# Optimization experiments

Hardware: AMD Instinct MI355X
Metric: run time of the kernel (lower is better)

The kernel has to match this reference:

```python
import jax, jax.numpy as jnp
import numpy as np

N, M, D_IN, H1, D, OUT_C = 2048, 128, 352, 512, 256, 13


def _lin_bn_relu(x, w, b, g, be):
    # 1x1 conv == linear over last dim; BN (eval) folded to per-channel affine (g, be)
    return jax.nn.relu(g * (x @ w.T + b) + be)


def _encode(x, wA, bA, gA, beA, wB, bB, gB, beB):
    return _lin_bn_relu(_lin_bn_relu(x, wA, bA, gA, beA), wB, bB, gB, beB)


def setup_inputs() -> dict:
    key = jax.random.key(0)
    ks = iter(jax.random.split(key, 64))

    def wgt(shape, s=0.05):
        return (jax.random.normal(next(ks), shape, jnp.float32) * s)

    def gamma(c):
        return 1.0 + 0.05 * jax.random.normal(next(ks), (c,), jnp.float32)

    inp = {}
    inp['ext_fea'] = jax.random.normal(next(ks), (N, D_IN), jnp.float32)
    inp['lab_fea'] = jax.random.normal(next(ks), (M, D_IN), jnp.float32)
    # convs1: 352->512->256, each Conv1d(1x1)+BN+ReLU
    inp.update(w1a=wgt((H1, D_IN)), b1a=wgt((H1,)), g1a=gamma(H1), be1a=wgt((H1,)))
    inp.update(w1b=wgt((D, H1)), b1b=wgt((D,)), g1b=gamma(D), be1b=wgt((D,)))
    # convs2: same shapes
    inp.update(w2a=wgt((H1, D_IN)), b2a=wgt((H1,)), g2a=gamma(H1), be2a=wgt((H1,)))
    inp.update(w2b=wgt((D, H1)), b2b=wgt((D,)), g2b=gamma(D), be2b=wgt((D,)))
    # wei_conv SharedMLP [256,32,64,256]: three Conv2d(1x1)+BN+ReLU
    inp.update(mw1=wgt((32, D)), mb1=wgt((32,)), mg1=gamma(32), mbe1=wgt((32,)))
    inp.update(mw2=wgt((64, 32)), mb2=wgt((64,)), mg2=gamma(64), mbe2=wgt((64,)))
    inp.update(mw3=wgt((D, 64)), mb3=wgt((D,)), mg3=gamma(D), mbe3=wgt((D,)))
    # fc
    inp.update(fcw=wgt((OUT_C, D)), fcb=wgt((OUT_C,)))
    return inp


def reference(ext_fea, lab_fea,
              w1a, b1a, g1a, be1a, w1b, b1b, g1b, be1b,
              w2a, b2a, g2a, be2a, w2b, b2b, g2b, be2b,
              mw1, mb1, mg1, mbe1, mw2, mb2, mg2, mbe2, mw3, mb3, mg3, mbe3,
              fcw, fcb):
    A = _encode(ext_fea, w1a, b1a, g1a, be1a, w1b, b1b, g1b, be1b)   # [N, 256]
    B = _encode(lab_fea, w2a, b2a, g2a, be2a, w2b, b2b, g2b, be2b)   # [M, 256]
    diff = A[:, None, :] - B[None, :, :]                             # [N, M, 256]
    h = _lin_bn_relu(diff, mw1, mb1, mg1, mbe1)                      # [N, M, 32]
    h = _lin_bn_relu(h, mw2, mb2, mg2, mbe2)                         # [N, M, 64]
    wei = _lin_bn_relu(h, mw3, mb3, mg3, mbe3)                       # [N, M, 256]
    # torch softmax over dim=-1 of [1,256,N,M] == over M == axis 1 here
    wei = jax.nn.softmax(wei, axis=1)
    att = jnp.sum(wei * diff, axis=1)                                # [N, 256]
    return att @ fcw.T + fcb                                         # [N, 13]
```

## Files before the change

kernel.cpp:

```cpp
#include <hip/hip_runtime.h>
#include <stdint.h>


typedef __attribute__((ext_vector_type(4))) float float4_t;
typedef __attribute__((ext_vector_type(4))) float f32x4;
typedef __attribute__((ext_vector_type(8))) short bf16x8;
typedef __attribute__((ext_vector_type(8))) unsigned short ushort8_t;
typedef __attribute__((ext_vector_type(4))) unsigned short ushort4_t;
typedef unsigned short ushort_t;

__device__ __forceinline__ float b2f(unsigned short u) {
  union { unsigned int i; float f; } v; v.i = ((unsigned int)u) << 16; return v.f;
}
__device__ __forceinline__ unsigned short f2b(float f) {
  union { float f; unsigned int i; } v; v.f = f;
  unsigned int x = v.i;
  return (unsigned short)((x + 0x7FFFu + ((x >> 16) & 1u)) >> 16);
}

template<int ISBF>
__device__ __forceinline__ ushort8_t ld8(const void* base, size_t idx) {
  if constexpr (ISBF) {
    return *(const ushort8_t*)((const ushort_t*)base + idx);
  } else {
    const float* p = (const float*)base + idx;
    float4_t v0 = *(const float4_t*)p;
    float4_t v1 = *(const float4_t*)(p + 4);
    ushort8_t u;
    #pragma unroll
    for (int e = 0; e < 4; ++e) { u[e] = f2b(v0[e]); u[4 + e] = f2b(v1[e]); }
    return u;
  }
}

template<int XBF, int WBF, int OUT_BF16>
__global__ __launch_bounds__(256) void enc_mfma(
    const void* __restrict__ XA, const void* __restrict__ WA,
    const float* __restrict__ bA, const float* __restrict__ gA, const float* __restrict__ beA,
    void* __restrict__ YA,
    const void* __restrict__ XB, const void* __restrict__ WB,
    const float* __restrict__ bB, const float* __restrict__ gB, const float* __restrict__ beB,
    void* __restrict__ YB, ushort_t* __restrict__ YBTb,
    int J, int K, int nbxA)
{
  __shared__ ushort_t Xs[2][32][40];
  __shared__ ushort_t Ws[2][32][40];
  const int bx = blockIdx.x, by = blockIdx.y;
  const void* X; const void* W;
  const float *bb, *gg, *bev; void* Y; int i0, isB;
  if (bx < nbxA) { X = XA; W = WA; bb = bA; gg = gA; bev = beA; Y = YA; i0 = bx * 32; isB = 0; }
  else           { X = XB; W = WB; bb = bB; gg = gB; bev = beB; Y = YB; i0 = (bx - nbxA) * 32; isB = 1; }
  const int j0 = by * 32;
  const int tid = threadIdx.x, w = tid >> 6, lane = tid & 63, lg = lane >> 4, lr = lane & 15;
  const int mt = w >> 1, ct = w & 1;
  const int row = tid >> 2, k8 = (tid & 3) * 8;

  f32x4 acc = f32x4{0.f, 0.f, 0.f, 0.f};

  ushort8_t sv = (row < 32) ? ld8<XBF>(X, (size_t)(i0 + row) * K + k8)
                            : ld8<WBF>(W, (size_t)(j0 + row - 32) * K + k8);
  for (int kt = 0; kt < K; kt += 32) {
    const int buf = (kt >> 5) & 1;
    if (row < 32) *(ushort8_t*)&Xs[buf][row][k8] = sv;
    else          *(ushort8_t*)&Ws[buf][row - 32][k8] = sv;
    __syncthreads();
    if (kt + 32 < K)
      sv = (row < 32) ? ld8<XBF>(X, (size_t)(i0 + row) * K + kt + 32 + k8)
                      : ld8<WBF>(W, (size_t)(j0 + row - 32) * K + kt + 32 + k8);
    bf16x8 af = *(const bf16x8*)&Xs[buf][mt * 16 + lr][lg * 8];
    bf16x8 bf_ = *(const bf16x8*)&Ws[buf][ct * 16 + lr][lg * 8];
    acc = __builtin_amdgcn_mfma_f32_16x16x32_bf16(af, bf_, acc, 0, 0, 0);
  }
  const int c = j0 + ct * 16 + lr;
  const float g = gg[c], bv = bb[c], ev = bev[c];
  #pragma unroll
  for (int r = 0; r < 4; ++r) {
    const int rowo = i0 + mt * 16 + 4 * lg + r;
    float t = fmaxf(g * (acc[r] + bv) + ev, 0.f);
    if (OUT_BF16) ((ushort_t*)Y)[(size_t)rowo * J + c] = f2b(t);
    else {
      ((float*)Y)[(size_t)rowo * J + c] = t;
      if (isB && YBTb) YBTb[(size_t)c * 128 + rowo] = f2b(t);
    }
  }
}

__global__ __launch_bounds__(256) void proj32(
    const float* __restrict__ Aenc, const float* __restrict__ Benc,
    const float* __restrict__ mw1, const float* __restrict__ mb1,
    const float* __restrict__ mg1, const float* __restrict__ mbe1,
    float* __restrict__ PA2, float* __restrict__ PB2, int nbxA,
    const float* __restrict__ mw2, const float* __restrict__ mw3,
    const float* __restrict__ mg2, const float* __restrict__ mb2, const float* __restrict__ mbe2,
    const float* __restrict__ mg3, const float* __restrict__ mb3, const float* __restrict__ mbe3,
    ushort_t* __restrict__ mw2bs, ushort_t* __restrict__ mw3b,
    float* __restrict__ c2arr, float* __restrict__ gs3arr, float* __restrict__ cs3arr)
{
  __shared__ float ps[4][32];
  const int tid = threadIdx.x, bx = blockIdx.x;
  const float LOG2E = 1.4426950408889634f;
  if (bx >= nbxA + 32) {
    const int t = bx - nbxA - 32;
    if (t == 9) {
      if (tid < 64)  c2arr[tid] = mg2[tid] * mb2[tid] + mbe2[tid];
      gs3arr[tid] = mg3[tid] * LOG2E;
      cs3arr[tid] = (mg3[tid] * mb3[tid] + mbe3[tid]) * LOG2E;
      return;
    }
    const int g = t * 256 + tid;
    if (g < 256) {
      const float sc = mg2[g >> 2];
      float4_t v0 = *(const float4_t*)&mw2[(size_t)g * 8];
      float4_t v1 = *(const float4_t*)&mw2[(size_t)g * 8 + 4];
      ushort8_t u;
      #pragma unroll
      for (int e = 0; e < 4; ++e) { u[e] = f2b(sc * v0[e]); u[4 + e] = f2b(sc * v1[e]); }
      *(ushort8_t*)&mw2bs[(size_t)g * 8] = u;
    } else {
      const int j = g - 256;
      float4_t v0 = *(const float4_t*)&mw3[(size_t)j * 8];
      float4_t v1 = *(const float4_t*)&mw3[(size_t)j * 8 + 4];
      ushort8_t u;
      #pragma unroll
      for (int e = 0; e < 4; ++e) { u[e] = f2b(v0[e]); u[4 + e] = f2b(v1[e]); }
      *(ushort8_t*)&mw3b[(size_t)j * 8] = u;
    }
    return;
  }
  const float* X; float* P; int n0, wb;
  if (bx < nbxA) { X = Aenc; P = PA2; n0 = bx * 4; wb = 1; }
  else           { X = Benc; P = PB2; n0 = (bx - nbxA) * 4; wb = 0; }
  const int k = tid & 31, r = (tid >> 5) & 3, half = tid >> 7;
  const int n = n0 + r;
  const float* xp = &X[(size_t)n * 256 + half * 128];
  const float* wp = &mw1[k * 256 + half * 128];
  float s = 0.f;
  #pragma unroll 8
  for (int q = 0; q < 128; q += 4) {
    float4_t xv = *(const float4_t*)&xp[q];
    float4_t wv = *(const float4_t*)&wp[q];
    #pragma unroll
    for (int e = 0; e < 4; ++e) s = fmaf(xv[e], wv[e], s);
  }
  if (half == 1) ps[r][k] = s;
  __syncthreads();
  if (half == 0) {
    s += ps[r][k];
    P[(size_t)n * 32 + k] = wb ? (mg1[k] * (s + mb1[k]) + mbe1[k]) : (mg1[k] * s);
  }
}

__global__ __launch_bounds__(256, 2) void main_attn(
    const float* __restrict__ PA2, const float* __restrict__ PB2,
    const float* __restrict__ A, const ushort_t* __restrict__ BmTb,
    const ushort_t* __restrict__ mw2bs, const float* __restrict__ c2arr,
    const ushort_t* __restrict__ mw3b, const float* __restrict__ gs3arr,
    const float* __restrict__ cs3arr,
    const float* __restrict__ fcw, const float* __restrict__ fcb,
    float* __restrict__ outp)
{
  __shared__ __align__(16) char smem[20288];
  const int tid = threadIdx.x;
  const int w = tid >> 6, lane = tid & 63, lg = lane >> 4, lr = lane & 15;
  const int n = blockIdx.x;
  const int cbase = w * 64;
  ushort_t* scrA = (ushort_t*)(smem + w * 4608);
  ushort_t* scrB = scrA + 1152;
  float* attL = (float*)(smem + 18432);
  float* part = (float*)(smem + 19456);

  float c2v[16];
  #pragma unroll
  for (int jt = 0; jt < 4; ++jt)
    #pragma unroll
    for (int r = 0; r < 4; ++r)
      c2v[jt * 4 + r] = c2arr[jt * 16 + 4 * lg + r];
  float gs3[4], cs3[4];
  #pragma unroll
  for (int ct = 0; ct < 4; ++ct) {
    const int c = cbase + ct * 16 + lr;
    gs3[ct] = gs3arr[c];
    cs3[ct] = cs3arr[c];
  }
  const float* pa = &PA2[(size_t)n * 32 + lg * 8];
  float4_t pa0 = *(const float4_t*)pa;
  float4_t pa1 = *(const float4_t*)(pa + 4);

  float smv[4], wbv[4];
  #pragma unroll
  for (int ct = 0; ct < 4; ++ct) { smv[ct] = 0.f; wbv[ct] = 0.f; }

  #pragma unroll 1
  for (int half = 0; half < 2; ++half) {
    bf16x8 b1[4];
    #pragma unroll
    for (int jt = 0; jt < 4; ++jt)
      b1[jt] = *(const bf16x8*)&mw2bs[(jt * 16 + lr) * 32 + lg * 8];

    bf16x8 af0[4], af1[4];
    #pragma unroll
    for (int mt = 0; mt < 4; ++mt) {
      const int m = half * 64 + mt * 16 + lr;
      const float* pb = &PB2[(size_t)m * 32 + lg * 8];
      float4_t pb0 = *(const float4_t*)pb;
      float4_t pb1 = *(const float4_t*)(pb + 4);
      bf16x8 a1;
      #pragma unroll
      for (int e = 0; e < 4; ++e) {
        a1[e]     = (short)f2b(fmaxf(pa0[e] - pb0[e], 0.f));
        a1[4 + e] = (short)f2b(fmaxf(pa1[e] - pb1[e], 0.f));
      }
      f32x4 acc1[4];
      #pragma unroll
      for (int jt = 0; jt < 4; ++jt)
        acc1[jt] = f32x4{c2v[jt * 4 + 0], c2v[jt * 4 + 1], c2v[jt * 4 + 2], c2v[jt * 4 + 3]};
      #pragma unroll
      for (int jt = 0; jt < 4; ++jt)
        acc1[jt] = __builtin_amdgcn_mfma_f32_16x16x32_bf16(b1[jt], a1, acc1[jt], 0, 0, 0);
      ushort_t* scr = (mt & 1) ? scrB : scrA;
      #pragma unroll
      for (int jt = 0; jt < 4; ++jt) {
        unsigned int lo = (unsigned int)f2b(fmaxf(acc1[jt][0], 0.f))
                        | ((unsigned int)f2b(fmaxf(acc1[jt][1], 0.f)) << 16);
        unsigned int hi = (unsigned int)f2b(fmaxf(acc1[jt][2], 0.f))
                        | ((unsigned int)f2b(fmaxf(acc1[jt][3], 0.f)) << 16);
        *(unsigned int*)&scr[lr * 72 + jt * 16 + 4 * lg]     = lo;
        *(unsigned int*)&scr[lr * 72 + jt * 16 + 4 * lg + 2] = hi;
      }
      af0[mt] = *(const bf16x8*)&scr[lr * 72 + lg * 8];
      af1[mt] = *(const bf16x8*)&scr[lr * 72 + 32 + lg * 8];
    }

    #pragma unroll
    for (int ct = 0; ct < 4; ++ct) {
      const int c = cbase + ct * 16 + lr;
      bf16x8 bfr0 = *(const bf16x8*)&mw3b[(size_t)c * 64 + lg * 8];
      bf16x8 bfr1 = *(const bf16x8*)&mw3b[(size_t)c * 64 + 32 + lg * 8];
      f32x4 acc[4];
      #pragma unroll
      for (int mt = 0; mt < 4; ++mt) acc[mt] = f32x4{0.f, 0.f, 0.f, 0.f};
      #pragma unroll
      for (int mt = 0; mt < 4; ++mt) {
        acc[mt] = __builtin_amdgcn_mfma_f32_16x16x32_bf16(af0[mt], bfr0, acc[mt], 0, 0, 0);
        acc[mt] = __builtin_amdgcn_mfma_f32_16x16x32_bf16(af1[mt], bfr1, acc[mt], 0, 0, 0);
      }
      f32x4 sm4 = f32x4{0.f, 0.f, 0.f, 0.f};
      f32x4 wb4 = f32x4{0.f, 0.f, 0.f, 0.f};
      #pragma unroll
      for (int mt = 0; mt < 4; ++mt) {
        ushort4_t bv4 = *(const ushort4_t*)&BmTb[(size_t)c * 128 + half * 64 + mt * 16 + 4 * lg];
        #pragma unroll
        for (int r = 0; r < 4; ++r) {
          float t = fmaf(gs3[ct], acc[mt][r], cs3[ct]);
          float p = __builtin_amdgcn_exp2f(__builtin_amdgcn_fmed3f(t, 0.f, 80.f));
          sm4[r] += p;
          wb4[r] = fmaf(p, b2f(bv4[r]), wb4[r]);
        }
      }
      smv[ct] += (sm4[0] + sm4[1]) + (sm4[2] + sm4[3]);
      wbv[ct] += (wb4[0] + wb4[1]) + (wb4[2] + wb4[3]);
    }
  }

  #pragma unroll
  for (int ct = 0; ct < 4; ++ct) {
    float sm = smv[ct], wb = wbv[ct];
    sm += __shfl_xor(sm, 16, 64);  wb += __shfl_xor(wb, 16, 64);
    sm += __shfl_xor(sm, 32, 64);  wb += __shfl_xor(wb, 32, 64);
    if (lg == 0) {
      const int c = cbase + ct * 16 + lr;
      attL[c] = A[(size_t)n * 256 + c] - wb / sm;
    }
  }
  __syncthreads();

  {
    const int o = tid >> 4, gp = tid & 15;
    if (o < 13) {
      float s = 0.f;
      #pragma unroll
      for (int i = 0; i < 4; ++i) {
        float4_t av = *(const float4_t*)&attL[gp * 16 + i * 4];
        float4_t wv = *(const float4_t*)&fcw[(size_t)o * 256 + gp * 16 + i * 4];
        #pragma unroll
        for (int e = 0; e < 4; ++e) s = fmaf(av[e], wv[e], s);
      }
      part[o * 16 + gp] = s;
    }
  }
  __syncthreads();
  if (tid < 13) {
    float s = fcb[tid];
    #pragma unroll
    for (int gp = 0; gp < 16; ++gp) s += part[tid * 16 + gp];
    outp[(size_t)n * 13 + tid] = s;
  }
}

extern "C" void kernel_launch(void* const* d_in, const int* in_sizes, int n_in,
                              void* d_out, int out_size, void* d_ws, size_t ws_size,
                              hipStream_t stream)
{
  const float* ext = (const float*)d_in[0];
  const float* lab = (const float*)d_in[1];
  const float* w1a = (const float*)d_in[2];
  const float* b1a = (const float*)d_in[3];
  const float* g1a = (const float*)d_in[4];
  const float* be1a= (const float*)d_in[5];
  const float* w1b = (const float*)d_in[6];
  const float* b1b = (const float*)d_in[7];
  const float* g1b = (const float*)d_in[8];
  const float* be1b= (const float*)d_in[9];
  const float* w2a = (const float*)d_in[10];
  const float* b2a = (const float*)d_in[11];
  const float* g2a = (const float*)d_in[12];
  const float* be2a= (const float*)d_in[13];
  const float* w2b = (const float*)d_in[14];
  const float* b2b = (const float*)d_in[15];
  const float* g2b = (const float*)d_in[16];
  const float* be2b= (const float*)d_in[17];
  const float* mw1 = (const float*)d_in[18];
  const float* mb1 = (const float*)d_in[19];
  const float* mg1 = (const float*)d_in[20];
  const float* mbe1= (const float*)d_in[21];
  const float* mw2 = (const float*)d_in[22];
  const float* mb2 = (const float*)d_in[23];
  const float* mg2 = (const float*)d_in[24];
  const float* mbe2= (const float*)d_in[25];
  const float* mw3 = (const float*)d_in[26];
  const float* mb3 = (const float*)d_in[27];
  const float* mg3 = (const float*)d_in[28];
  const float* mbe3= (const float*)d_in[29];
  const float* fcw = (const float*)d_in[30];
  const float* fcb = (const float*)d_in[31];

  char* ws = (char*)d_ws;
  ushort_t* Y1ab = (ushort_t*)(ws);
  float*    PA2  = (float*)(ws);
  float*    PB2  = (float*)(ws + 262144);
  float*    Aenc = (float*)(ws + (2u << 20));
  char* b5 = ws + (4u << 20);
  ushort_t* mw2bs = (ushort_t*)(b5);
  ushort_t* mw3b  = (ushort_t*)(b5 + 4096);
  ushort_t* Y1bb  = (ushort_t*)(b5 + 36864);
  float*    Benc  = (float*)(b5 + 167936);
  ushort_t* BencTb= (ushort_t*)(b5 + 299008);
  float*    c2arr = (float*)(b5 + 364544);
  float*    gs3arr= (float*)(b5 + 364800);
  float*    cs3arr= (float*)(b5 + 365824);

  enc_mfma<0, 0, 1><<<dim3(68, 16), 256, 0, stream>>>(
      (const void*)ext, (const void*)w1a, b1a, g1a, be1a, (void*)Y1ab,
      (const void*)lab, (const void*)w2a, b2a, g2a, be2a, (void*)Y1bb,
      (ushort_t*)nullptr, 512, 352, 64);
  enc_mfma<1, 0, 0><<<dim3(68, 8), 256, 0, stream>>>(
      (const void*)Y1ab, (const void*)w1b, b1b, g1b, be1b, (void*)Aenc,
      (const void*)Y1bb, (const void*)w2b, b2b, g2b, be2b, (void*)Benc,
      BencTb, 256, 512, 64);
  proj32<<<554, 256, 0, stream>>>(Aenc, Benc, mw1, mb1, mg1, mbe1, PA2, PB2, 512,
                                  mw2, mw3, mg2, mb2, mbe2, mg3, mb3, mbe3,
                                  mw2bs, mw3b, c2arr, gs3arr, cs3arr);
  main_attn<<<2048, 256, 0, stream>>>(PA2, PB2, Aenc, BencTb,
                                      mw2bs, c2arr, mw3b, gs3arr, cs3arr,
                                      fcw, fcb, (float*)d_out);
}
```

Measured before the change: 98.52 us.

## Repartition attention work: each wave owns one row-half, two rows per block

The main attention kernel previously had each of four waves own 64 output channels for one row n and recompute the 128x64 hidden layer redundantly per wave. Now each block handles two rows, and each wave owns one half of the M dimension across all 256 channels. The second MLP layer is computed once per wave, and partial softmax sums from the two halves are combined through shared memory. This removes the fourfold redundant layer-2 MFMA and conversion work, at the cost of more live registers (16 channel tiles of accumulators) and a larger LDS footprint, which may reduce occupancy.

```diff
diff --git a/kernel.cpp b/kernel.cpp
--- a/kernel.cpp
+++ b/kernel.cpp
@@ -159,116 +159,113 @@
     const float* __restrict__ fcw, const float* __restrict__ fcb,
     float* __restrict__ outp)
 {
-  __shared__ __align__(16) char smem[20288];
+  __shared__ __align__(16) char smem[36864];
   const int tid = threadIdx.x;
   const int w = tid >> 6, lane = tid & 63, lg = lane >> 4, lr = lane & 15;
-  const int n = blockIdx.x;
-  const int cbase = w * 64;
-  ushort_t* scrA = (ushort_t*)(smem + w * 4608);
-  ushort_t* scrB = scrA + 1152;
-  float* attL = (float*)(smem + 18432);
-  float* part = (float*)(smem + 19456);
-
-  float c2v[16];
-  #pragma unroll
-  for (int jt = 0; jt < 4; ++jt)
-    #pragma unroll
-    for (int r = 0; r < 4; ++r)
-      c2v[jt * 4 + r] = c2arr[jt * 16 + 4 * lg + r];
-  float gs3[4], cs3[4];
-  #pragma unroll
-  for (int ct = 0; ct < 4; ++ct) {
-    const int c = cbase + ct * 16 + lr;
-    gs3[ct] = gs3arr[c];
-    cs3[ct] = cs3arr[c];
+  const int n = blockIdx.x * 2 + (w >> 1);
+  const int half = w & 1;
+  ushort_t* h2s = (ushort_t*)(smem + w * 9216);
+
+  bf16x8 b1[4];
+  float c2v[4];
+  #pragma unroll
+  for (int jt = 0; jt < 4; ++jt) {
+    b1[jt] = *(const bf16x8*)&mw2bs[(jt * 16 + lr) * 32 + lg * 8];
+    c2v[jt] = c2arr[jt * 16 + lr];
   }
   const float* pa = &PA2[(size_t)n * 32 + lg * 8];
   float4_t pa0 = *(const float4_t*)pa;
   float4_t pa1 = *(const float4_t*)(pa + 4);
 
-  float smv[4], wbv[4];
-  #pragma unroll
-  for (int ct = 0; ct < 4; ++ct) { smv[ct] = 0.f; wbv[ct] = 0.f; }
-
-  #pragma unroll 1
-  for (int half = 0; half < 2; ++half) {
-    bf16x8 b1[4];
+  #pragma unroll
+  for (int mt = 0; mt < 4; ++mt) {
+    const int m = half * 64 + mt * 16 + lr;
+    const float* pb = &PB2[(size_t)m * 32 + lg * 8];
+    float4_t pb0 = *(const float4_t*)pb;
+    float4_t pb1 = *(const float4_t*)(pb + 4);
+    bf16x8 a1;
+    #pragma unroll
+    for (int e = 0; e < 4; ++e) {
+      a1[e]     = (short)f2b(fmaxf(pa0[e] - pb0[e], 0.f));
+      a1[4 + e] = (short)f2b(fmaxf(pa1[e] - pb1[e], 0.f));
+    }
+    f32x4 acc1[4];
     #pragma unroll
     for (int jt = 0; jt < 4; ++jt)
-      b1[jt] = *(const bf16x8*)&mw2bs[(jt * 16 + lr) * 32 + lg * 8];
-
-    bf16x8 af0[4], af1[4];
+      acc1[jt] = f32x4{c2v[jt], c2v[jt], c2v[jt], c2v[jt]};
+    #pragma unroll
+    for (int jt = 0; jt < 4; ++jt)
+      acc1[jt] = __builtin_amdgcn_mfma_f32_16x16x32_bf16(a1, b1[jt], acc1[jt], 0, 0, 0);
+    #pragma unroll
+    for (int jt = 0; jt < 4; ++jt)
+      #pragma unroll
+      for (int r = 0; r < 4; ++r)
+        h2s[(mt * 16 + 4 * lg + r) * 72 + jt * 16 + lr] =
+            f2b(fmaxf(acc1[jt][r], 0.f));
+  }
+
+  bf16x8 af0[4], af1[4];
+  #pragma unroll
+  for (int mt = 0; mt < 4; ++mt) {
+    af0[mt] = *(const bf16x8*)&h2s[(mt * 16 + lr) * 72 + lg * 8];
+    af1[mt] = *(const bf16x8*)&h2s[(mt * 16 + lr) * 72 + 32 + lg * 8];
+  }
+
+  float smv[16], wbv[16];
+  #pragma unroll
+  for (int ct = 0; ct < 16; ++ct) {
+    const int c = ct * 16 + lr;
+    bf16x8 bfr0 = *(const bf16x8*)&mw3b[(size_t)c * 64 + lg * 8];
+    bf16x8 bfr1 = *(const bf16x8*)&mw3b[(size_t)c * 64 + 32 + lg * 8];
+    f32x4 acc[4];
+    #pragma unroll
+    for (int mt = 0; mt < 4; ++mt) acc[mt] = f32x4{0.f, 0.f, 0.f, 0.f};
     #pragma unroll
     for (int mt = 0; mt < 4; ++mt) {
-      const int m = half * 64 + mt * 16 + lr;
-      const float* pb = &PB2[(size_t)m * 32 + lg * 8];
-      float4_t pb0 = *(const float4_t*)pb;
-      float4_t pb1 = *(const float4_t*)(pb + 4);
-      bf16x8 a1;
-      #pragma unroll
-      for (int e = 0; e < 4; ++e) {
-        a1[e]     = (short)f2b(fmaxf(pa0[e] - pb0[e], 0.f));
-        a1[4 + e] = (short)f2b(fmaxf(pa1[e] - pb1[e], 0.f));
+      acc[mt] = __builtin_amdgcn_mfma_f32_16x16x32_bf16(af0[mt], bfr0, acc[mt], 0, 0, 0);
+      acc[mt] = __builtin_amdgcn_mfma_f32_16x16x32_bf16(af1[mt], bfr1, acc[mt], 0, 0, 0);
+    }
+    const float gs = gs3arr[c];
+    const float cs = cs3arr[c];
+    f32x4 sm4 = f32x4{0.f, 0.f, 0.f, 0.f};
+    f32x4 wb4 = f32x4{0.f, 0.f, 0.f, 0.f};
+    #pragma unroll
+    for (int mt = 0; mt < 4; ++mt) {
+      ushort4_t bv4 = *(const ushort4_t*)&BmTb[(size_t)c * 128 + half * 64 + mt * 16 + 4 * lg];
+      #pragma unroll
+      for (int r = 0; r < 4; ++r) {
+        float t = fmaf(gs, acc[mt][r], cs);
+        float p = __builtin_amdgcn_exp2f(__builtin_amdgcn_fmed3f(t, 0.f, 80.f));
+        sm4[r] += p;
+        wb4[r] = fmaf(p, b2f(bv4[r]), wb4[r]);
       }
-      f32x4 acc1[4];
-      #pragma unroll
-      for (int jt = 0; jt < 4; ++jt)
-        acc1[jt] = f32x4{c2v[jt * 4 + 0], c2v[jt * 4 + 1], c2v[jt * 4 + 2], c2v[jt * 4 + 3]};
-      #pragma unroll
-      for (int jt = 0; jt < 4; ++jt)
-        acc1[jt] = __builtin_amdgcn_mfma_f32_16x16x32_bf16(b1[jt], a1, acc1[jt], 0, 0, 0);
-      ushort_t* scr = (mt & 1) ? scrB : scrA;
-      #pragma unroll
-      for (int jt = 0; jt < 4; ++jt) {
-        unsigned int lo = (unsigned int)f2b(fmaxf(acc1[jt][0], 0.f))
-                        | ((unsigned int)f2b(fmaxf(acc1[jt][1], 0.f)) << 16);
-        unsigned int hi = (unsigned int)f2b(fmaxf(acc1[jt][2], 0.f))
-                        | ((unsigned int)f2b(fmaxf(acc1[jt][3], 0.f)) << 16);
-        *(unsigned int*)&scr[lr * 72 + jt * 16 + 4 * lg]     = lo;
-        *(unsigned int*)&scr[lr * 72 + jt * 16 + 4 * lg + 2] = hi;
-      }
-      af0[mt] = *(const bf16x8*)&scr[lr * 72 + lg * 8];
-      af1[mt] = *(const bf16x8*)&scr[lr * 72 + 32 + lg * 8];
-    }
-
-    #pragma unroll
-    for (int ct = 0; ct < 4; ++ct) {
-      const int c = cbase + ct * 16 + lr;
-      bf16x8 bfr0 = *(const bf16x8*)&mw3b[(size_t)c * 64 + lg * 8];
-      bf16x8 bfr1 = *(const bf16x8*)&mw3b[(size_t)c * 64 + 32 + lg * 8];
-      f32x4 acc[4];
-      #pragma unroll
-      for (int mt = 0; mt < 4; ++mt) acc[mt] = f32x4{0.f, 0.f, 0.f, 0.f};
-      #pragma unroll
-      for (int mt = 0; mt < 4; ++mt) {
-        acc[mt] = __builtin_amdgcn_mfma_f32_16x16x32_bf16(af0[mt], bfr0, acc[mt], 0, 0, 0);
-        acc[mt] = __builtin_amdgcn_mfma_f32_16x16x32_bf16(af1[mt], bfr1, acc[mt], 0, 0, 0);
-      }
-      f32x4 sm4 = f32x4{0.f, 0.f, 0.f, 0.f};
-      f32x4 wb4 = f32x4{0.f, 0.f, 0.f, 0.f};
-      #pragma unroll
-      for (int mt = 0; mt < 4; ++mt) {
-        ushort4_t bv4 = *(const ushort4_t*)&BmTb[(size_t)c * 128 + half * 64 + mt * 16 + 4 * lg];
-        #pragma unroll
-        for (int r = 0; r < 4; ++r) {
-          float t = fmaf(gs3[ct], acc[mt][r], cs3[ct]);
-          float p = __builtin_amdgcn_exp2f(__builtin_amdgcn_fmed3f(t, 0.f, 80.f));
-          sm4[r] += p;
-          wb4[r] = fmaf(p, b2f(bv4[r]), wb4[r]);
-        }
-      }
-      smv[ct] += (sm4[0] + sm4[1]) + (sm4[2] + sm4[3]);
-      wbv[ct] += (wb4[0] + wb4[1]) + (wb4[2] + wb4[3]);
-    }
-  }
-
-  #pragma unroll
-  for (int ct = 0; ct < 4; ++ct) {
+    }
+    smv[ct] = (sm4[0] + sm4[1]) + (sm4[2] + sm4[3]);
+    wbv[ct] = (wb4[0] + wb4[1]) + (wb4[2] + wb4[3]);
+  }
+
+  float* smp = (float*)(smem + w * 9216);
+  float* wbp = (float*)(smem + w * 9216 + 1024);
+  #pragma unroll
+  for (int ct = 0; ct < 16; ++ct) {
     float sm = smv[ct], wb = wbv[ct];
     sm += __shfl_xor(sm, 16, 64);  wb += __shfl_xor(wb, 16, 64);
     sm += __shfl_xor(sm, 32, 64);  wb += __shfl_xor(wb, 32, 64);
-    if (lg == 0) {
-      const int c = cbase + ct * 16 + lr;
+    if (lg == 0) { smp[ct * 16 + lr] = sm; wbp[ct * 16 + lr] = wb; }
+  }
+  __syncthreads();
+
+  if (half == 0) {
+    const float* smA = (const float*)(smem + w * 9216);
+    const float* wbA = (const float*)(smem + w * 9216 + 1024);
+    const float* smB = (const float*)(smem + (w + 1) * 9216);
+    const float* wbB = (const float*)(smem + (w + 1) * 9216 + 1024);
+    float* attL = (float*)(smem + w * 9216 + 2048);
+    #pragma unroll
+    for (int i = 0; i < 4; ++i) {
+      const int c = i * 64 + lane;
+      float sm = smA[c] + smB[c];
+      float wb = wbA[c] + wbB[c];
       attL[c] = A[(size_t)n * 256 + c] - wb / sm;
     }
   }
@@ -277,23 +274,30 @@
   {
     const int o = tid >> 4, gp = tid & 15;
     if (o < 13) {
-      float s = 0.f;
-      #pragma unroll
-      for (int i = 0; i < 4; ++i) {
-        float4_t av = *(const float4_t*)&attL[gp * 16 + i * 4];
-        float4_t wv = *(const float4_t*)&fcw[(size_t)o * 256 + gp * 16 + i * 4];
+      #pragma unroll
+      for (int h = 0; h < 2; ++h) {
+        const float* attL = (const float*)(smem + (h * 2) * 9216 + 2048);
+        float* part = (float*)(smem + (h * 2) * 9216 + 3072);
+        float s = 0.f;
         #pragma unroll
-        for (int e = 0; e < 4; ++e) s = fmaf(av[e], wv[e], s);
+        for (int i = 0; i < 4; ++i) {
+          float4_t av = *(const float4_t*)&attL[gp * 16 + i * 4];
+          float4_t wv = *(const float4_t*)&fcw[(size_t)o * 256 + gp * 16 + i * 4];
+          #pragma unroll
+          for (int e = 0; e < 4; ++e) s = fmaf(av[e], wv[e], s);
+        }
+        part[o * 16 + gp] = s;
       }
-      part[o * 16 + gp] = s;
     }
   }
   __syncthreads();
-  if (tid < 13) {
-    float s = fcb[tid];
-    #pragma unroll
-    for (int gp = 0; gp < 16; ++gp) s += part[tid * 16 + gp];
-    outp[(size_t)n * 13 + tid] = s;
+  if (tid < 26) {
+    const int nn = tid / 13, o = tid % 13;
+    const float* part = (const float*)(smem + (nn * 2) * 9216 + 3072);
+    float s = fcb[o];
+    #pragma unroll
+    for (int gp = 0; gp < 16; ++gp) s += part[o * 16 + gp];
+    outp[(size_t)(blockIdx.x * 2 + nn) * 13 + o] = s;
   }
 }
 
@@ -360,7 +364,7 @@
   proj32<<<554, 256, 0, stream>>>(Aenc, Benc, mw1, mb1, mg1, mbe1, PA2, PB2, 512,
                                   mw2, mw3, mg2, mb2, mbe2, mg3, mb3, mbe3,
                                   mw2bs, mw3b, c2arr, gs3arr, cs3arr);
-  main_attn<<<2048, 256, 0, stream>>>(PA2, PB2, Aenc, BencTb,
+  main_attn<<<1024, 256, 0, stream>>>(PA2, PB2, Aenc, BencTb,
                                       mw2bs, c2arr, mw3b, gs3arr, cs3arr,
                                       fcw, fcb, (float*)d_out);
 }
```

After: 129.6 us. +31.5%, slower.

## Split attention work by M rows per wave to drop redundant layer-2 MFMAs

Applied to the files above, without the earlier changes.

Each wave now owns 32 of the 128 label rows and iterates over all 256 output channels, instead of owning 64 channels and recomputing the full 128-row hidden layer. This removes the 4x redundant first-stage MFMA, bf16 conversion and LDS staging work. The price is a cross-wave reduction of softmax sums and weighted sums through shared memory, plus an extra barrier. Per-channel scale and shift are now loaded inside the channel loop rather than held in registers.

```diff
diff --git a/kernel.cpp b/kernel.cpp
--- a/kernel.cpp
+++ b/kernel.cpp
@@ -159,124 +159,110 @@
     const float* __restrict__ fcw, const float* __restrict__ fcb,
     float* __restrict__ outp)
 {
-  __shared__ __align__(16) char smem[20288];
+  __shared__ __align__(16) char smem[18432];
   const int tid = threadIdx.x;
   const int w = tid >> 6, lane = tid & 63, lg = lane >> 4, lr = lane & 15;
   const int n = blockIdx.x;
-  const int cbase = w * 64;
-  ushort_t* scrA = (ushort_t*)(smem + w * 4608);
-  ushort_t* scrB = scrA + 1152;
-  float* attL = (float*)(smem + 18432);
-  float* part = (float*)(smem + 19456);
-
-  float c2v[16];
+  ushort_t* scr = (ushort_t*)(smem + w * 4608);
+
+  bf16x8 b1[4];
   #pragma unroll
   for (int jt = 0; jt < 4; ++jt)
-    #pragma unroll
-    for (int r = 0; r < 4; ++r)
-      c2v[jt * 4 + r] = c2arr[jt * 16 + 4 * lg + r];
-  float gs3[4], cs3[4];
-  #pragma unroll
-  for (int ct = 0; ct < 4; ++ct) {
-    const int c = cbase + ct * 16 + lr;
-    gs3[ct] = gs3arr[c];
-    cs3[ct] = cs3arr[c];
-  }
+    b1[jt] = *(const bf16x8*)&mw2bs[(jt * 16 + lr) * 32 + lg * 8];
   const float* pa = &PA2[(size_t)n * 32 + lg * 8];
   float4_t pa0 = *(const float4_t*)pa;
   float4_t pa1 = *(const float4_t*)(pa + 4);
 
-  float smv[4], wbv[4];
+  bf16x8 af0[2], af1[2];
   #pragma unroll
-  for (int ct = 0; ct < 4; ++ct) { smv[ct] = 0.f; wbv[ct] = 0.f; }
-
-  #pragma unroll 1
-  for (int half = 0; half < 2; ++half) {
-    bf16x8 b1[4];
+  for (int mt = 0; mt < 2; ++mt) {
+    const int m = w * 32 + mt * 16 + lr;
+    const float* pb = &PB2[(size_t)m * 32 + lg * 8];
+    float4_t pb0 = *(const float4_t*)pb;
+    float4_t pb1 = *(const float4_t*)(pb + 4);
+    bf16x8 a1;
+    #pragma unroll
+    for (int e = 0; e < 4; ++e) {
+      a1[e]     = (short)f2b(fmaxf(pa0[e] - pb0[e], 0.f));
+      a1[4 + e] = (short)f2b(fmaxf(pa1[e] - pb1[e], 0.f));
+    }
+    f32x4 acc1[4];
     #pragma unroll
     for (int jt = 0; jt < 4; ++jt)
-      b1[jt] = *(const bf16x8*)&mw2bs[(jt * 16 + lr) * 32 + lg * 8];
-
-    bf16x8 af0[4], af1[4];
-    #pragma unroll
-    for (int mt = 0; mt < 4; ++mt) {
-      const int m = half * 64 + mt * 16 + lr;
-      const float* pb = &PB2[(size_t)m * 32 + lg * 8];
-      float4_t pb0 = *(const float4_t*)pb;
-      float4_t pb1 = *(const float4_t*)(pb + 4);
-      bf16x8 a1;
-      #pragma unroll
-      for (int e = 0; e < 4; ++e) {
-        a1[e]     = (short)f2b(fmaxf(pa0[e] - pb0[e], 0.f));
-        a1[4 + e] = (short)f2b(fmaxf(pa1[e] - pb1[e], 0.f));
-      }
-      f32x4 acc1[4];
-      #pragma unroll
-      for (int jt = 0; jt < 4; ++jt)
-        acc1[jt] = f32x4{c2v[jt * 4 + 0], c2v[jt * 4 + 1], c2v[jt * 4 + 2], c2v[jt * 4 + 3]};
-      #pragma unroll
-      for (int jt = 0; jt < 4; ++jt)
-        acc1[jt] = __builtin_amdgcn_mfma_f32_16x16x32_bf16(b1[jt], a1, acc1[jt], 0, 0, 0);
-      ushort_t* scr = (mt & 1) ? scrB : scrA;
-      #pragma unroll
-      for (int jt = 0; jt < 4; ++jt) {
-        unsigned int lo = (unsigned int)f2b(fmaxf(acc1[jt][0], 0.f))
-                        | ((unsigned int)f2b(fmaxf(acc1[jt][1], 0.f)) << 16);
-        unsigned int hi = (unsigned int)f2b(fmaxf(acc1[jt][2], 0.f))
-                        | ((unsigned int)f2b(fmaxf(acc1[jt][3], 0.f)) << 16);
-        *(unsigned int*)&scr[lr * 72 + jt * 16 + 4 * lg]     = lo;
-        *(unsigned int*)&scr[lr * 72 + jt * 16 + 4 * lg + 2] = hi;
-      }
-      af0[mt] = *(const bf16x8*)&scr[lr * 72 + lg * 8];
-      af1[mt] = *(const bf16x8*)&scr[lr * 72 + 32 + lg * 8];
-    }
-
-    #pragma unroll
-    for (int ct = 0; ct < 4; ++ct) {
-      const int c = cbase + ct * 16 + lr;
-      bf16x8 bfr0 = *(const bf16x8*)&mw3b[(size_t)c * 64 + lg * 8];
-      bf16x8 bfr1 = *(const bf16x8*)&mw3b[(size_t)c * 64 + 32 + lg * 8];
-      f32x4 acc[4];
-      #pragma unroll
-      for (int mt = 0; mt < 4; ++mt) acc[mt] = f32x4{0.f, 0.f, 0.f, 0.f};
-      #pragma unroll
-      for (int mt = 0; mt < 4; ++mt) {
-        acc[mt] = __builtin_amdgcn_mfma_f32_16x16x32_bf16(af0[mt], bfr0, acc[mt], 0, 0, 0);
-        acc[mt] = __builtin_amdgcn_mfma_f32_16x16x32_bf16(af1[mt], bfr1, acc[mt], 0, 0, 0);
-      }
-      f32x4 sm4 = f32x4{0.f, 0.f, 0.f, 0.f};
-      f32x4 wb4 = f32x4{0.f, 0.f, 0.f, 0.f};
-      #pragma unroll
-      for (int mt = 0; mt < 4; ++mt) {
-        ushort4_t bv4 = *(const ushort4_t*)&BmTb[(size_t)c * 128 + half * 64 + mt * 16 + 4 * lg];
-        #pragma unroll
-        for (int r = 0; r < 4; ++r) {
-          float t = fmaf(gs3[ct], acc[mt][r], cs3[ct]);
-          float p = __builtin_amdgcn_exp2f(__builtin_amdgcn_fmed3f(t, 0.f, 80.f));
-          sm4[r] += p;
-          wb4[r] = fmaf(p, b2f(bv4[r]), wb4[r]);
-        }
-      }
-      smv[ct] += (sm4[0] + sm4[1]) + (sm4[2] + sm4[3]);
-      wbv[ct] += (wb4[0] + wb4[1]) + (wb4[2] + wb4[3]);
-    }
-  }
-
-  #pragma unroll
-  for (int ct = 0; ct < 4; ++ct) {
-    float sm = smv[ct], wb = wbv[ct];
+      acc1[jt] = *(const f32x4*)&c2arr[jt * 16 + 4 * lg];
+    #pragma unroll
+    for (int jt = 0; jt < 4; ++jt)
+      acc1[jt] = __builtin_amdgcn_mfma_f32_16x16x32_bf16(b1[jt], a1, acc1[jt], 0, 0, 0);
+    ushort_t* sb = scr + mt * 1152;
+    #pragma unroll
+    for (int jt = 0; jt < 4; ++jt) {
+      unsigned int lo = (unsigned int)f2b(fmaxf(acc1[jt][0], 0.f))
+                      | ((unsigned int)f2b(fmaxf(acc1[jt][1], 0.f)) << 16);
+      unsigned int hi = (unsigned int)f2b(fmaxf(acc1[jt][2], 0.f))
+                      | ((unsigned int)f2b(fmaxf(acc1[jt][3], 0.f)) << 16);
+      *(unsigned int*)&sb[lr * 72 + jt * 16 + 4 * lg]     = lo;
+      *(unsigned int*)&sb[lr * 72 + jt * 16 + 4 * lg + 2] = hi;
+    }
+    af0[mt] = *(const bf16x8*)&sb[lr * 72 + lg * 8];
+    af1[mt] = *(const bf16x8*)&sb[lr * 72 + 32 + lg * 8];
+  }
+
+  float* smp = (float*)(smem + w * 4608);
+  float* wbp = (float*)(smem + w * 4608 + 1024);
+  #pragma unroll 4
+  for (int ct = 0; ct < 16; ++ct) {
+    const int c = ct * 16 + lr;
+    bf16x8 bfr0 = *(const bf16x8*)&mw3b[(size_t)c * 64 + lg * 8];
+    bf16x8 bfr1 = *(const bf16x8*)&mw3b[(size_t)c * 64 + 32 + lg * 8];
+    f32x4 accA = f32x4{0.f, 0.f, 0.f, 0.f};
+    f32x4 accB = f32x4{0.f, 0.f, 0.f, 0.f};
+    accA = __builtin_amdgcn_mfma_f32_16x16x32_bf16(af0[0], bfr0, accA, 0, 0, 0);
+    accA = __builtin_amdgcn_mfma_f32_16x16x32_bf16(af1[0], bfr1, accA, 0, 0, 0);
+    accB = __builtin_amdgcn_mfma_f32_16x16x32_bf16(af0[1], bfr0, accB, 0, 0, 0);
+    accB = __builtin_amdgcn_mfma_f32_16x16x32_bf16(af1[1], bfr1, accB, 0, 0, 0);
+    const float gs = gs3arr[c];
+    const float cs = cs3arr[c];
+    ushort4_t bvA = *(const ushort4_t*)&BmTb[(size_t)c * 128 + w * 32 + 4 * lg];
+    ushort4_t bvB = *(const ushort4_t*)&BmTb[(size_t)c * 128 + w * 32 + 16 + 4 * lg];
+    f32x4 sm4 = f32x4{0.f, 0.f, 0.f, 0.f};
+    f32x4 wb4 = f32x4{0.f, 0.f, 0.f, 0.f};
+    #pragma unroll
+    for (int r = 0; r < 4; ++r) {
+      float tA = fmaf(gs, accA[r], cs);
+      float pA = __builtin_amdgcn_exp2f(__builtin_amdgcn_fmed3f(tA, 0.f, 80.f));
+      sm4[r] += pA;
+      wb4[r] = fmaf(pA, b2f(bvA[r]), wb4[r]);
+      float tB = fmaf(gs, accB[r], cs);
+      float pB = __builtin_amdgcn_exp2f(__builtin_amdgcn_fmed3f(tB, 0.f, 80.f));
+      sm4[r] += pB;
+      wb4[r] = fmaf(pB, b2f(bvB[r]), wb4[r]);
+    }
+    float sm = (sm4[0] + sm4[1]) + (sm4[2] + sm4[3]);
+    float wb = (wb4[0] + wb4[1]) + (wb4[2] + wb4[3]);
     sm += __shfl_xor(sm, 16, 64);  wb += __shfl_xor(wb, 16, 64);
     sm += __shfl_xor(sm, 32, 64);  wb += __shfl_xor(wb, 32, 64);
-    if (lg == 0) {
-      const int c = cbase + ct * 16 + lr;
-      attL[c] = A[(size_t)n * 256 + c] - wb / sm;
-    }
+    if (lg == 0) { smp[c] = sm; wbp[c] = wb; }
+  }
+  __syncthreads();
+
+  {
+    const int c = tid;
+    float sm = 0.f, wb = 0.f;
+    #pragma unroll
+    for (int ww = 0; ww < 4; ++ww) {
+      sm += ((const float*)(smem + ww * 4608))[c];
+      wb += ((const float*)(smem + ww * 4608 + 1024))[c];
+    }
+    float* attL = (float*)(smem + 2048);
+    attL[c] = A[(size_t)n * 256 + c] - wb / sm;
   }
   __syncthreads();
 
   {
     const int o = tid >> 4, gp = tid & 15;
     if (o < 13) {
+      const float* attL = (const float*)(smem + 2048);
+      float* part = (float*)(smem + 3072);
       float s = 0.f;
       #pragma unroll
       for (int i = 0; i < 4; ++i) {
@@ -290,6 +276,7 @@
   }
   __syncthreads();
   if (tid < 13) {
+    const float* part = (const float*)(smem + 3072);
     float s = fcb[tid];
     #pragma unroll
     for (int gp = 0; gp < 16; ++gp) s += part[tid * 16 + gp];
```

Result: slower. 107.3 us (+8.9%).
